# Kernel tuning notes

Hardware: AMD Instinct MI355X
Metric: run time of the kernel (lower is better)

The kernel has to match this reference:

```python
import jax, jax.numpy as jnp
import numpy as np

B, T, D, H = 2, 4096, 512, 8
DH = D // H  # dim_head = 64


def setup_inputs() -> dict:
    key = jax.random.key(0)
    ks = jax.random.split(key, 10)
    s = 1.0 / np.sqrt(D)
    x = jax.random.normal(ks[0], (B, T, D), dtype=jnp.float32)
    Wq = jax.random.uniform(ks[1], (D, D), jnp.float32, -s, s)
    Wk = jax.random.uniform(ks[2], (D, D), jnp.float32, -s, s)
    Wv = jax.random.uniform(ks[3], (D, D), jnp.float32, -s, s)
    Wo = jax.random.uniform(ks[4], (D, D), jnp.float32, -s, s)
    bq = jnp.zeros((D,), jnp.float32)
    bk = jnp.zeros((D,), jnp.float32)
    bv = jnp.zeros((D,), jnp.float32)
    bo = jnp.zeros((D,), jnp.float32)
    mask = jax.random.randint(ks[5], (1, 1, T, T), 0, 2).astype(bool)
    return {"x": x, "Wq": Wq, "bq": bq, "Wk": Wk, "bk": bk,
            "Wv": Wv, "bv": bv, "Wo": Wo, "bo": bo, "mask": mask}


def reference(x, Wq, bq, Wk, bk, Wv, bv, Wo, bo, mask):
    # QKV projections (self-attention: Q=K=V=x)
    def split_heads(t):
        return t.reshape(B, T, H, DH).transpose(0, 2, 1, 3)  # (B,H,T,DH)
    Q = split_heads(x @ Wq + bq)
    K = split_heads(x @ Wk + bk)
    V = split_heads(x @ Wv + bv)
    # scaled dot-product attention with additive mask penalty (as in source)
    scores = jnp.einsum('bhqd,bhkd->bhqk', Q, K) / np.sqrt(DH)
    scores = scores + (~mask).astype(scores.dtype) * (-1e9)
    att_w = jax.nn.softmax(scores, axis=-1)
    O = jnp.einsum('bhqk,bhkd->bhqd', att_w, V)
    O = O.transpose(0, 2, 1, 3).reshape(B, T, D)
    return O @ Wo + bo
```

## Files before the change

### kernel.cpp

```cpp
#include <hip/hip_runtime.h>
#include <stdint.h>

#define B_ 2
#define T_ 4096
#define D_ 512
#define H_ 8
#define DH_ 64

typedef __bf16 bf16;
typedef __bf16 bf16x4_t __attribute__((ext_vector_type(4)));
typedef __bf16 bf16x8_t __attribute__((ext_vector_type(8)));
typedef float f32x4 __attribute__((ext_vector_type(4)));
typedef uint32_t u32;

static constexpr float QSCALE = 0.18033688011112042f;

__device__ __forceinline__ void async16(void* lds, const void* g) {
  __builtin_amdgcn_global_load_lds(
      (const __attribute__((address_space(1))) void*)g,
      (__attribute__((address_space(3))) void*)lds, 16, 0, 0);
}

__global__ __launch_bounds__(256) void prep_kernel(
    const float* __restrict__ x,
    const float* __restrict__ Wq, const float* __restrict__ Wk,
    const float* __restrict__ Wv, const float* __restrict__ Wo,
    const void* __restrict__ maskp,
    bf16* __restrict__ xb, bf16* __restrict__ WTall, bf16* __restrict__ WoT,
    u32* __restrict__ bmask)
{
  int bid = blockIdx.x;
  int tid = threadIdx.x;
  if (bid < 4096) {
    int idx = bid * 256 + tid;
    const float4* xf = (const float4*)x;
    float4 v = xf[idx];
    bf16x4_t o;
    o[0] = (bf16)v.x; o[1] = (bf16)v.y; o[2] = (bf16)v.z; o[3] = (bf16)v.w;
    ((bf16x4_t*)xb)[idx] = o;
  } else if (bid < 8192) {
    int gid = (bid - 4096) * 256 + tid;
    int sel = gid >> 18;
    int idx = gid & 262143;
    int n = idx >> 9, k = idx & 511;
    if (sel < 3) {
      const float* W = (sel == 0) ? Wq : (sel == 1) ? Wk : Wv;
      float v = W[k * 512 + n];
      if (sel == 0) v *= QSCALE;
      WTall[gid] = (bf16)v;
    } else {
      WoT[idx] = (bf16)Wo[k * 512 + n];
    }
  } else {
    int wid = (bid - 8192) * 256 + tid;
    const uint8_t* m8 = (const uint8_t*)maskp;
    bool u8mode = (__ballot(m8[4 * (tid & 63) + 1] != 0) != 0ull);
    int row = wid >> 7, wcol = wid & 127;
    size_t off = (size_t)row * 4096 + (size_t)wcol * 32;
    u32 w = 0;
    if (u8mode) {
      const uint4* p = (const uint4*)(m8 + off);
      uint4 a = p[0], b = p[1];
      u32 ws[8] = {a.x, a.y, a.z, a.w, b.x, b.y, b.z, b.w};
      #pragma unroll
      for (int j = 0; j < 32; ++j)
        if ((ws[j >> 2] >> ((j & 3) * 8)) & 0xffu) w |= (1u << j);
    } else {
      const uint4* p = (const uint4*)((const u32*)maskp + off);
      #pragma unroll
      for (int q = 0; q < 8; ++q) {
        uint4 a = p[q];
        if (a.x) w |= 1u << (q * 4 + 0);
        if (a.y) w |= 1u << (q * 4 + 1);
        if (a.z) w |= 1u << (q * 4 + 2);
        if (a.w) w |= 1u << (q * 4 + 3);
      }
    }
    bmask[((size_t)(row >> 6) * 64 + (wcol >> 1)) * 128 + (row & 63) * 2 + (wcol & 1)] = w;
  }
}

__global__ __launch_bounds__(256) void qkv_kernel(
    const bf16* __restrict__ xb, const bf16* __restrict__ WTall,
    const float* __restrict__ bq, const float* __restrict__ bk,
    const float* __restrict__ bv,
    bf16* __restrict__ Qb, bf16* __restrict__ Kb, bf16* __restrict__ Vtb)
{
  __shared__ char smem[16384];
  char* smX = smem;
  char* smW = smem + 8192;
  int tid = threadIdx.x;
  int lane = tid & 63, wave = tid >> 6;
  int lo = lane & 15, quad = lane >> 4;
  int wr = wave >> 1, wc = wave & 1;
  int bm = blockIdx.x * 64;
  int bn = blockIdx.y * 64;
  int sel = bn >> 9;
  f32x4 acc[2][2] = {};
  for (int kc = 0; kc < 8; ++kc) {
    __syncthreads();
    for (int s = tid; s < 512; s += 256) {
      int row = s >> 3, slot = s & 7, cg = slot ^ (row & 7);
      async16(smX + s * 16, xb + (size_t)(bm + row) * 512 + kc * 64 + cg * 8);
      async16(smW + s * 16, WTall + (size_t)(bn + row) * 512 + kc * 64 + cg * 8);
    }
    __syncthreads();
    #pragma unroll
    for (int ks = 0; ks < 2; ++ks) {
      bf16x8_t a[2], b[2];
      #pragma unroll
      for (int mt = 0; mt < 2; ++mt) {
        int row = wr * 32 + mt * 16 + lo;
        int ch = (ks * 4 + quad) ^ (row & 7);
        a[mt] = *(const bf16x8_t*)(smX + row * 128 + ch * 16);
      }
      #pragma unroll
      for (int nt = 0; nt < 2; ++nt) {
        int row = wc * 32 + nt * 16 + lo;
        int ch = (ks * 4 + quad) ^ (row & 7);
        b[nt] = *(const bf16x8_t*)(smW + row * 128 + ch * 16);
      }
      if (sel == 2) {
        #pragma unroll
        for (int mt = 0; mt < 2; ++mt)
          #pragma unroll
          for (int nt = 0; nt < 2; ++nt)
            acc[mt][nt] = __builtin_amdgcn_mfma_f32_16x16x32_bf16(
                b[nt], a[mt], acc[mt][nt], 0, 0, 0);
      } else {
        #pragma unroll
        for (int mt = 0; mt < 2; ++mt)
          #pragma unroll
          for (int nt = 0; nt < 2; ++nt)
            acc[mt][nt] = __builtin_amdgcn_mfma_f32_16x16x32_bf16(
                a[mt], b[nt], acc[mt][nt], 0, 0, 0);
      }
    }
  }
  int b_ = bm >> 12;
  if (sel < 2) {
    #pragma unroll
    for (int mt = 0; mt < 2; ++mt) {
      #pragma unroll
      for (int nt = 0; nt < 2; ++nt) {
        int n0 = (bn + wc * 32 + nt * 16 + lo) & 511;
        int h = n0 >> 6, dh = n0 & 63;
        int m0 = bm + wr * 32 + mt * 16 + quad * 4;
        int t0 = m0 & 4095;
        float bias = (sel == 0) ? QSCALE * bq[n0] : bk[n0];
        bf16* dst = (sel == 0 ? Qb : Kb) + (size_t)(b_ * H_ + h) * T_ * DH_ + dh;
        #pragma unroll
        for (int r = 0; r < 4; ++r)
          dst[(size_t)(t0 + r) * 64] = (bf16)(acc[mt][nt][r] + bias);
      }
    }
  } else {
    #pragma unroll
    for (int mt = 0; mt < 2; ++mt) {
      #pragma unroll
      for (int nt = 0; nt < 2; ++nt) {
        int t0 = (bm & 4095) + wr * 32 + mt * 16 + lo;
        #pragma unroll
        for (int r = 0; r < 4; ++r) {
          int n0 = (bn & 511) + wc * 32 + nt * 16 + quad * 4 + r;
          float v = acc[mt][nt][r] + bv[n0];
          Vtb[((size_t)(b_ * H_ + (n0 >> 6)) * DH_ + (n0 & 63)) * T_ + t0] = (bf16)v;
        }
      }
    }
  }
}

__global__ __launch_bounds__(256, 4) void attn_kernel(
    const bf16* __restrict__ Qb, const bf16* __restrict__ Kb,
    const bf16* __restrict__ Vtb, const u32* __restrict__ bm2,
    bf16* __restrict__ Obuf)
{
  __shared__ char smem[27648];
  char* smK = smem;
  char* smV = smem + 8192;
  char* smP = smem + 16384;
  char* smM = smem + 26624;
  int tid = threadIdx.x;
  int lane = tid & 63, wave = tid >> 6;
  int lo = lane & 15, quad = lane >> 4;
  int qh = wave & 1, kh = wave >> 1;
  int bh = blockIdx.x >> 6;
  int qt = blockIdx.x & 63;
  int qbase = qt * 64;
  char* smPw = smP + wave * 2560;

  const bf16* Qg = Qb + ((size_t)bh * T_ + qbase + qh * 32) * DH_;
  bf16x8_t qf[2][2];
  #pragma unroll
  for (int mt = 0; mt < 2; ++mt)
    #pragma unroll
    for (int ks = 0; ks < 2; ++ks)
      qf[mt][ks] = *(const bf16x8_t*)(Qg + (mt * 16 + lo) * 64 + ks * 32 + quad * 8);

  f32x4 O[2][4] = {};
  float lsum[2][4] = {};

  const bf16* Kg = Kb + (size_t)bh * T_ * DH_;
  const bf16* Vg = Vtb + (size_t)bh * DH_ * T_;
  const u32* mg = bm2 + (size_t)qt * 8192;

  for (int kc = 0; kc < 64; ++kc) {
    __syncthreads();
    for (int s = tid; s < 512; s += 256) {
      int row = s >> 3, slot = s & 7, cg = slot ^ (row & 7);
      async16(smK + s * 16, Kg + (size_t)(kc * 64 + row) * 64 + cg * 8);
      async16(smV + s * 16, Vg + (size_t)row * T_ + kc * 64 + cg * 8);
    }
    if (tid < 128) ((u32*)smM)[tid] = mg[kc * 128 + tid];
    __syncthreads();
    f32x4 S[2][2] = {};
    #pragma unroll
    for (int ks = 0; ks < 2; ++ks)
      #pragma unroll
      for (int nt = 0; nt < 2; ++nt) {
        int key = kh * 32 + nt * 16 + lo;
        int ch = (ks * 4 + quad) ^ (key & 7);
        bf16x8_t kf = *(const bf16x8_t*)(smK + key * 128 + ch * 16);
        #pragma unroll
        for (int mt = 0; mt < 2; ++mt)
          S[mt][nt] = __builtin_amdgcn_mfma_f32_16x16x32_bf16(
              qf[mt][ks], kf, S[mt][nt], 0, 0, 0);
      }
    #pragma unroll
    for (int mt = 0; mt < 2; ++mt)
      #pragma unroll
      for (int r = 0; r < 4; ++r) {
        int q_l = qh * 32 + mt * 16 + quad * 4 + r;
        u32 w = (*(const u32*)(smM + (q_l * 2 + kh) * 4)) >> lo;
        int prow = mt * 16 + quad * 4 + r;
        #pragma unroll
        for (int nt = 0; nt < 2; ++nt) {
          float p = __builtin_amdgcn_exp2f(S[mt][nt][r]);
          p = ((w >> (nt * 16)) & 1u) ? p : 0.0f;
          lsum[mt][r] += p;
          *(bf16*)(smPw + prow * 80 + (nt * 16 + lo) * 2) = (bf16)p;
        }
      }
    bf16x8_t pf[2];
    #pragma unroll
    for (int mt = 0; mt < 2; ++mt)
      pf[mt] = *(const bf16x8_t*)(smPw + (mt * 16 + lo) * 80 + quad * 16);
    #pragma unroll
    for (int dt = 0; dt < 4; ++dt) {
      int d = dt * 16 + lo;
      int ch = (kh * 4 + quad) ^ (d & 7);
      bf16x8_t vf = *(const bf16x8_t*)(smV + d * 128 + ch * 16);
      #pragma unroll
      for (int mt = 0; mt < 2; ++mt)
        O[mt][dt] = __builtin_amdgcn_mfma_f32_16x16x32_bf16(
            pf[mt], vf, O[mt][dt], 0, 0, 0);
    }
  }
  #pragma unroll
  for (int mt = 0; mt < 2; ++mt)
    #pragma unroll
    for (int r = 0; r < 4; ++r) {
      float v = lsum[mt][r];
      v += __shfl_xor(v, 1); v += __shfl_xor(v, 2);
      v += __shfl_xor(v, 4); v += __shfl_xor(v, 8);
      lsum[mt][r] = v;
    }
  __syncthreads();
  float* smO = (float*)smem;
  float* smL = (float*)smP;
  if (kh == 1) {
    #pragma unroll
    for (int mt = 0; mt < 2; ++mt) {
      #pragma unroll
      for (int dt = 0; dt < 4; ++dt)
        #pragma unroll
        for (int r = 0; r < 4; ++r)
          smO[(qh * 32 + mt * 16 + quad * 4 + r) * 64 + dt * 16 + lo] = O[mt][dt][r];
      if (lo == 0)
        #pragma unroll
        for (int r = 0; r < 4; ++r)
          smL[qh * 32 + mt * 16 + quad * 4 + r] = lsum[mt][r];
    }
  }
  __syncthreads();
  if (kh == 0) {
    bf16* Og = Obuf + ((size_t)bh * T_ + qbase + qh * 32) * DH_;
    #pragma unroll
    for (int mt = 0; mt < 2; ++mt) {
      float inv[4];
      #pragma unroll
      for (int r = 0; r < 4; ++r) {
        int row = qh * 32 + mt * 16 + quad * 4 + r;
        inv[r] = 1.0f / (lsum[mt][r] + smL[row]);
      }
      #pragma unroll
      for (int dt = 0; dt < 4; ++dt)
        #pragma unroll
        for (int r = 0; r < 4; ++r) {
          int rl = mt * 16 + quad * 4 + r;
          float o = (O[mt][dt][r] + smO[(qh * 32 + rl) * 64 + dt * 16 + lo]) * inv[r];
          Og[(size_t)rl * 64 + dt * 16 + lo] = (bf16)o;
        }
    }
  }
}

__global__ __launch_bounds__(256) void proj_kernel(
    const bf16* __restrict__ Obuf, const bf16* __restrict__ WoT,
    const float* __restrict__ bo, float* __restrict__ out)
{
  __shared__ char smem[16384];
  char* smA = smem;
  char* smW = smem + 8192;
  int tid = threadIdx.x;
  int lane = tid & 63, wave = tid >> 6;
  int lo = lane & 15, quad = lane >> 4;
  int wr = wave >> 1, wc = wave & 1;
  int bm = blockIdx.x * 64;
  int bn = blockIdx.y * 64;
  int b_ = bm >> 12, trow = bm & 4095;
  f32x4 acc[2][2] = {};
  for (int kc = 0; kc < 8; ++kc) {
    __syncthreads();
    const bf16* Ag = Obuf + ((size_t)(b_ * H_ + kc) * T_ + trow) * DH_;
    for (int s = tid; s < 512; s += 256) {
      int row = s >> 3, slot = s & 7, cg = slot ^ (row & 7);
      async16(smA + s * 16, Ag + row * 64 + cg * 8);
      async16(smW + s * 16, WoT + (size_t)(bn + row) * 512 + kc * 64 + cg * 8);
    }
    __syncthreads();
    #pragma unroll
    for (int ks = 0; ks < 2; ++ks) {
      bf16x8_t a[2], b[2];
      #pragma unroll
      for (int mt = 0; mt < 2; ++mt) {
        int row = wr * 32 + mt * 16 + lo;
        int ch = (ks * 4 + quad) ^ (row & 7);
        a[mt] = *(const bf16x8_t*)(smA + row * 128 + ch * 16);
      }
      #pragma unroll
      for (int nt = 0; nt < 2; ++nt) {
        int row = wc * 32 + nt * 16 + lo;
        int ch = (ks * 4 + quad) ^ (row & 7);
        b[nt] = *(const bf16x8_t*)(smW + row * 128 + ch * 16);
      }
      #pragma unroll
      for (int mt = 0; mt < 2; ++mt)
        #pragma unroll
        for (int nt = 0; nt < 2; ++nt)
          acc[mt][nt] = __builtin_amdgcn_mfma_f32_16x16x32_bf16(
              a[mt], b[nt], acc[mt][nt], 0, 0, 0);
    }
  }
  #pragma unroll
  for (int mt = 0; mt < 2; ++mt) {
    #pragma unroll
    for (int nt = 0; nt < 2; ++nt) {
      int n_g = bn + wc * 32 + nt * 16 + lo;
      int m0 = bm + wr * 32 + mt * 16 + quad * 4;
      float bias = bo[n_g];
      #pragma unroll
      for (int r = 0; r < 4; ++r)
        out[(size_t)(m0 + r) * 512 + n_g] = acc[mt][nt][r] + bias;
    }
  }
}

extern "C" void kernel_launch(void* const* d_in, const int* in_sizes, int n_in,
                              void* d_out, int out_size, void* d_ws, size_t ws_size,
                              hipStream_t stream) {
  const float* x  = (const float*)d_in[0];
  const float* Wq = (const float*)d_in[1];
  const float* bq = (const float*)d_in[2];
  const float* Wk = (const float*)d_in[3];
  const float* bk = (const float*)d_in[4];
  const float* Wv = (const float*)d_in[5];
  const float* bv = (const float*)d_in[6];
  const float* Wo = (const float*)d_in[7];
  const float* bo = (const float*)d_in[8];
  const void* maskp = d_in[9];
  float* out = (float*)d_out;

  char* w = (char*)d_ws;
  bf16* xb    = (bf16*)(w);
  bf16* WTall = (bf16*)(w + 8388608);
  bf16* WoT   = (bf16*)(w + 9961472);
  bf16* Qb    = (bf16*)(w + 10485760);
  bf16* Kb    = (bf16*)(w + 18874368);
  bf16* Vtb   = (bf16*)(w + 27262976);
  bf16* Obuf  = (bf16*)(w + 35651584);
  u32*  bmask = (u32*)(w + 44040192);

  prep_kernel<<<10240, 256, 0, stream>>>(x, Wq, Wk, Wv, Wo, maskp,
                                         xb, WTall, WoT, bmask);
  qkv_kernel<<<dim3(128, 24), 256, 0, stream>>>(xb, WTall, bq, bk, bv,
                                                Qb, Kb, Vtb);
  attn_kernel<<<1024, 256, 0, stream>>>(Qb, Kb, Vtb, bmask, Obuf);
  proj_kernel<<<dim3(128, 8), 256, 0, stream>>>(Obuf, WoT, bo, out);
}
```

Before: 305.5 us.

## Keep attention probabilities in registers via transposed S; enlarge GEMM tiles to 128x128

The attention kernel now computes S transposed (K as the A operand), so each lane's exp results already sit in the layout the 16x16x16 MFMA expects for the P·V product. This removes the per-wave LDS round trip for P and makes the mask load asynchronous. Row-sum reduction and the cross-wave combine are reworked to match. The QKV and output projection GEMMs grow from 64x64 to 128x128 block tiles with 4x4 MFMA tiles per wave, which gives more reuse per load but launches fewer blocks and uses more registers.

```diff
diff --git a/kernel.cpp b/kernel.cpp
--- a/kernel.cpp
+++ b/kernel.cpp
@@ -11,6 +11,7 @@
 typedef __bf16 bf16x4_t __attribute__((ext_vector_type(4)));
 typedef __bf16 bf16x8_t __attribute__((ext_vector_type(8)));
 typedef float f32x4 __attribute__((ext_vector_type(4)));
+typedef short short4_t __attribute__((ext_vector_type(4)));
 typedef uint32_t u32;
 
 static constexpr float QSCALE = 0.18033688011112042f;
@@ -86,20 +87,20 @@
     const float* __restrict__ bv,
     bf16* __restrict__ Qb, bf16* __restrict__ Kb, bf16* __restrict__ Vtb)
 {
-  __shared__ char smem[16384];
+  __shared__ char smem[32768];
   char* smX = smem;
-  char* smW = smem + 8192;
+  char* smW = smem + 16384;
   int tid = threadIdx.x;
   int lane = tid & 63, wave = tid >> 6;
   int lo = lane & 15, quad = lane >> 4;
   int wr = wave >> 1, wc = wave & 1;
-  int bm = blockIdx.x * 64;
-  int bn = blockIdx.y * 64;
+  int bm = blockIdx.x * 128;
+  int bn = blockIdx.y * 128;
   int sel = bn >> 9;
-  f32x4 acc[2][2] = {};
+  f32x4 acc[4][4] = {};
   for (int kc = 0; kc < 8; ++kc) {
     __syncthreads();
-    for (int s = tid; s < 512; s += 256) {
+    for (int s = tid; s < 1024; s += 256) {
       int row = s >> 3, slot = s & 7, cg = slot ^ (row & 7);
       async16(smX + s * 16, xb + (size_t)(bm + row) * 512 + kc * 64 + cg * 8);
       async16(smW + s * 16, WTall + (size_t)(bn + row) * 512 + kc * 64 + cg * 8);
@@ -107,31 +108,31 @@
     __syncthreads();
     #pragma unroll
     for (int ks = 0; ks < 2; ++ks) {
-      bf16x8_t a[2], b[2];
-      #pragma unroll
-      for (int mt = 0; mt < 2; ++mt) {
-        int row = wr * 32 + mt * 16 + lo;
+      bf16x8_t a[4], b[4];
+      #pragma unroll
+      for (int mt = 0; mt < 4; ++mt) {
+        int row = wr * 64 + mt * 16 + lo;
         int ch = (ks * 4 + quad) ^ (row & 7);
         a[mt] = *(const bf16x8_t*)(smX + row * 128 + ch * 16);
       }
       #pragma unroll
-      for (int nt = 0; nt < 2; ++nt) {
-        int row = wc * 32 + nt * 16 + lo;
+      for (int nt = 0; nt < 4; ++nt) {
+        int row = wc * 64 + nt * 16 + lo;
         int ch = (ks * 4 + quad) ^ (row & 7);
         b[nt] = *(const bf16x8_t*)(smW + row * 128 + ch * 16);
       }
       if (sel == 2) {
         #pragma unroll
-        for (int mt = 0; mt < 2; ++mt)
+        for (int mt = 0; mt < 4; ++mt)
           #pragma unroll
-          for (int nt = 0; nt < 2; ++nt)
+          for (int nt = 0; nt < 4; ++nt)
             acc[mt][nt] = __builtin_amdgcn_mfma_f32_16x16x32_bf16(
                 b[nt], a[mt], acc[mt][nt], 0, 0, 0);
       } else {
         #pragma unroll
-        for (int mt = 0; mt < 2; ++mt)
+        for (int mt = 0; mt < 4; ++mt)
           #pragma unroll
-          for (int nt = 0; nt < 2; ++nt)
+          for (int nt = 0; nt < 4; ++nt)
             acc[mt][nt] = __builtin_amdgcn_mfma_f32_16x16x32_bf16(
                 a[mt], b[nt], acc[mt][nt], 0, 0, 0);
       }
@@ -140,12 +141,12 @@
   int b_ = bm >> 12;
   if (sel < 2) {
     #pragma unroll
-    for (int mt = 0; mt < 2; ++mt) {
-      #pragma unroll
-      for (int nt = 0; nt < 2; ++nt) {
-        int n0 = (bn + wc * 32 + nt * 16 + lo) & 511;
+    for (int mt = 0; mt < 4; ++mt) {
+      #pragma unroll
+      for (int nt = 0; nt < 4; ++nt) {
+        int n0 = (bn + wc * 64 + nt * 16 + lo) & 511;
         int h = n0 >> 6, dh = n0 & 63;
-        int m0 = bm + wr * 32 + mt * 16 + quad * 4;
+        int m0 = bm + wr * 64 + mt * 16 + quad * 4;
         int t0 = m0 & 4095;
         float bias = (sel == 0) ? QSCALE * bq[n0] : bk[n0];
         bf16* dst = (sel == 0 ? Qb : Kb) + (size_t)(b_ * H_ + h) * T_ * DH_ + dh;
@@ -156,13 +157,13 @@
     }
   } else {
     #pragma unroll
-    for (int mt = 0; mt < 2; ++mt) {
-      #pragma unroll
-      for (int nt = 0; nt < 2; ++nt) {
-        int t0 = (bm & 4095) + wr * 32 + mt * 16 + lo;
+    for (int mt = 0; mt < 4; ++mt) {
+      #pragma unroll
+      for (int nt = 0; nt < 4; ++nt) {
+        int t0 = (bm & 4095) + wr * 64 + mt * 16 + lo;
         #pragma unroll
         for (int r = 0; r < 4; ++r) {
-          int n0 = (bn & 511) + wc * 32 + nt * 16 + quad * 4 + r;
+          int n0 = (bn & 511) + wc * 64 + nt * 16 + quad * 4 + r;
           float v = acc[mt][nt][r] + bv[n0];
           Vtb[((size_t)(b_ * H_ + (n0 >> 6)) * DH_ + (n0 & 63)) * T_ + t0] = (bf16)v;
         }
@@ -176,34 +177,32 @@
     const bf16* __restrict__ Vtb, const u32* __restrict__ bm2,
     bf16* __restrict__ Obuf)
 {
-  __shared__ char smem[27648];
+  __shared__ char smem[16896];
   char* smK = smem;
   char* smV = smem + 8192;
-  char* smP = smem + 16384;
-  char* smM = smem + 26624;
+  u32* smM = (u32*)(smem + 16384);
   int tid = threadIdx.x;
   int lane = tid & 63, wave = tid >> 6;
   int lo = lane & 15, quad = lane >> 4;
   int qh = wave & 1, kh = wave >> 1;
   int bh = blockIdx.x >> 6;
-  int qt = blockIdx.x & 63;
-  int qbase = qt * 64;
-  char* smPw = smP + wave * 2560;
+  int qt64 = blockIdx.x & 63;
+  int qbase = qt64 * 64;
 
   const bf16* Qg = Qb + ((size_t)bh * T_ + qbase + qh * 32) * DH_;
   bf16x8_t qf[2][2];
   #pragma unroll
-  for (int mt = 0; mt < 2; ++mt)
+  for (int qt = 0; qt < 2; ++qt)
     #pragma unroll
     for (int ks = 0; ks < 2; ++ks)
-      qf[mt][ks] = *(const bf16x8_t*)(Qg + (mt * 16 + lo) * 64 + ks * 32 + quad * 8);
+      qf[qt][ks] = *(const bf16x8_t*)(Qg + (qt * 16 + lo) * 64 + ks * 32 + quad * 8);
 
   f32x4 O[2][4] = {};
-  float lsum[2][4] = {};
+  float lsum[2] = {0.f, 0.f};
 
   const bf16* Kg = Kb + (size_t)bh * T_ * DH_;
   const bf16* Vg = Vtb + (size_t)bh * DH_ * T_;
-  const u32* mg = bm2 + (size_t)qt * 8192;
+  const u32* mg = bm2 + (size_t)qt64 * 8192;
 
   for (int kc = 0; kc < 64; ++kc) {
     __syncthreads();
@@ -212,96 +211,95 @@
       async16(smK + s * 16, Kg + (size_t)(kc * 64 + row) * 64 + cg * 8);
       async16(smV + s * 16, Vg + (size_t)row * T_ + kc * 64 + cg * 8);
     }
-    if (tid < 128) ((u32*)smM)[tid] = mg[kc * 128 + tid];
-    __syncthreads();
-    f32x4 S[2][2] = {};
+    if (tid < 32) async16((char*)smM + tid * 16, mg + kc * 128 + tid * 4);
+    __syncthreads();
+    f32x4 St[2][2] = {};
     #pragma unroll
     for (int ks = 0; ks < 2; ++ks)
       #pragma unroll
-      for (int nt = 0; nt < 2; ++nt) {
-        int key = kh * 32 + nt * 16 + lo;
-        int ch = (ks * 4 + quad) ^ (key & 7);
-        bf16x8_t kf = *(const bf16x8_t*)(smK + key * 128 + ch * 16);
-        #pragma unroll
-        for (int mt = 0; mt < 2; ++mt)
-          S[mt][nt] = __builtin_amdgcn_mfma_f32_16x16x32_bf16(
-              qf[mt][ks], kf, S[mt][nt], 0, 0, 0);
-      }
-    #pragma unroll
-    for (int mt = 0; mt < 2; ++mt)
-      #pragma unroll
-      for (int r = 0; r < 4; ++r) {
-        int q_l = qh * 32 + mt * 16 + quad * 4 + r;
-        u32 w = (*(const u32*)(smM + (q_l * 2 + kh) * 4)) >> lo;
-        int prow = mt * 16 + quad * 4 + r;
-        #pragma unroll
-        for (int nt = 0; nt < 2; ++nt) {
-          float p = __builtin_amdgcn_exp2f(S[mt][nt][r]);
-          p = ((w >> (nt * 16)) & 1u) ? p : 0.0f;
-          lsum[mt][r] += p;
-          *(bf16*)(smPw + prow * 80 + (nt * 16 + lo) * 2) = (bf16)p;
+      for (int kt = 0; kt < 2; ++kt) {
+        int krow = kh * 32 + kt * 16 + lo;
+        int ch = (ks * 4 + quad) ^ (krow & 7);
+        bf16x8_t kf = *(const bf16x8_t*)(smK + krow * 128 + ch * 16);
+        #pragma unroll
+        for (int qt = 0; qt < 2; ++qt)
+          St[kt][qt] = __builtin_amdgcn_mfma_f32_16x16x32_bf16(
+              kf, qf[qt][ks], St[kt][qt], 0, 0, 0);
+      }
+    short4_t pf[2][2];
+    #pragma unroll
+    for (int qt = 0; qt < 2; ++qt) {
+      u32 w = smM[(qh * 32 + qt * 16 + lo) * 2 + kh] >> (quad * 4);
+      #pragma unroll
+      for (int kt = 0; kt < 2; ++kt) {
+        bf16x4_t t;
+        #pragma unroll
+        for (int r = 0; r < 4; ++r) {
+          float p = ((w >> (kt * 16 + r)) & 1u)
+                        ? __builtin_amdgcn_exp2f(St[kt][qt][r]) : 0.0f;
+          lsum[qt] += p;
+          t[r] = (bf16)p;
         }
-      }
-    bf16x8_t pf[2];
-    #pragma unroll
-    for (int mt = 0; mt < 2; ++mt)
-      pf[mt] = *(const bf16x8_t*)(smPw + (mt * 16 + lo) * 80 + quad * 16);
+        pf[qt][kt] = __builtin_bit_cast(short4_t, t);
+      }
+    }
     #pragma unroll
     for (int dt = 0; dt < 4; ++dt) {
       int d = dt * 16 + lo;
-      int ch = (kh * 4 + quad) ^ (d & 7);
-      bf16x8_t vf = *(const bf16x8_t*)(smV + d * 128 + ch * 16);
-      #pragma unroll
-      for (int mt = 0; mt < 2; ++mt)
-        O[mt][dt] = __builtin_amdgcn_mfma_f32_16x16x32_bf16(
-            pf[mt], vf, O[mt][dt], 0, 0, 0);
+      #pragma unroll
+      for (int kt = 0; kt < 2; ++kt) {
+        int c0 = kh * 4 + kt * 2 + (quad >> 1);
+        short4_t vf = *(const short4_t*)(
+            smV + d * 128 + ((c0 ^ (d & 7)) << 4) + ((quad & 1) << 3));
+        #pragma unroll
+        for (int qt = 0; qt < 2; ++qt)
+          O[qt][dt] = __builtin_amdgcn_mfma_f32_16x16x16bf16_1k(
+              pf[qt][kt], vf, O[qt][dt], 0, 0, 0);
+      }
     }
   }
   #pragma unroll
-  for (int mt = 0; mt < 2; ++mt)
-    #pragma unroll
-    for (int r = 0; r < 4; ++r) {
-      float v = lsum[mt][r];
-      v += __shfl_xor(v, 1); v += __shfl_xor(v, 2);
-      v += __shfl_xor(v, 4); v += __shfl_xor(v, 8);
-      lsum[mt][r] = v;
-    }
+  for (int qt = 0; qt < 2; ++qt) {
+    float v = lsum[qt];
+    v += __shfl_xor(v, 16);
+    v += __shfl_xor(v, 32);
+    lsum[qt] = v;
+  }
   __syncthreads();
   float* smO = (float*)smem;
-  float* smL = (float*)smP;
+  float* smL = (float*)(smem + 16384);
   if (kh == 1) {
     #pragma unroll
-    for (int mt = 0; mt < 2; ++mt) {
+    for (int qt = 0; qt < 2; ++qt) {
       #pragma unroll
       for (int dt = 0; dt < 4; ++dt)
         #pragma unroll
         for (int r = 0; r < 4; ++r)
-          smO[(qh * 32 + mt * 16 + quad * 4 + r) * 64 + dt * 16 + lo] = O[mt][dt][r];
-      if (lo == 0)
-        #pragma unroll
-        for (int r = 0; r < 4; ++r)
-          smL[qh * 32 + mt * 16 + quad * 4 + r] = lsum[mt][r];
-    }
+          smO[(qh * 32 + qt * 16 + quad * 4 + r) * 64 + dt * 16 + lo] = O[qt][dt][r];
+      if (quad == 0) smL[qh * 32 + qt * 16 + lo] = lsum[qt];
+    }
+  }
+  __syncthreads();
+  if (kh == 0 && quad == 0) {
+    #pragma unroll
+    for (int qt = 0; qt < 2; ++qt)
+      smL[qh * 32 + qt * 16 + lo] += lsum[qt];
   }
   __syncthreads();
   if (kh == 0) {
     bf16* Og = Obuf + ((size_t)bh * T_ + qbase + qh * 32) * DH_;
     #pragma unroll
-    for (int mt = 0; mt < 2; ++mt) {
-      float inv[4];
+    for (int qt = 0; qt < 2; ++qt) {
       #pragma unroll
       for (int r = 0; r < 4; ++r) {
-        int row = qh * 32 + mt * 16 + quad * 4 + r;
-        inv[r] = 1.0f / (lsum[mt][r] + smL[row]);
-      }
-      #pragma unroll
-      for (int dt = 0; dt < 4; ++dt)
-        #pragma unroll
-        for (int r = 0; r < 4; ++r) {
-          int rl = mt * 16 + quad * 4 + r;
-          float o = (O[mt][dt][r] + smO[(qh * 32 + rl) * 64 + dt * 16 + lo]) * inv[r];
+        int rl = qt * 16 + quad * 4 + r;
+        float inv = 1.0f / smL[qh * 32 + rl];
+        #pragma unroll
+        for (int dt = 0; dt < 4; ++dt) {
+          float o = (O[qt][dt][r] + smO[(qh * 32 + rl) * 64 + dt * 16 + lo]) * inv;
           Og[(size_t)rl * 64 + dt * 16 + lo] = (bf16)o;
         }
+      }
     }
   }
 }
@@ -310,21 +308,21 @@
     const bf16* __restrict__ Obuf, const bf16* __restrict__ WoT,
     const float* __restrict__ bo, float* __restrict__ out)
 {
-  __shared__ char smem[16384];
+  __shared__ char smem[32768];
   char* smA = smem;
-  char* smW = smem + 8192;
+  char* smW = smem + 16384;
   int tid = threadIdx.x;
   int lane = tid & 63, wave = tid >> 6;
   int lo = lane & 15, quad = lane >> 4;
   int wr = wave >> 1, wc = wave & 1;
-  int bm = blockIdx.x * 64;
-  int bn = blockIdx.y * 64;
+  int bm = blockIdx.x * 128;
+  int bn = blockIdx.y * 128;
   int b_ = bm >> 12, trow = bm & 4095;
-  f32x4 acc[2][2] = {};
+  f32x4 acc[4][4] = {};
   for (int kc = 0; kc < 8; ++kc) {
     __syncthreads();
     const bf16* Ag = Obuf + ((size_t)(b_ * H_ + kc) * T_ + trow) * DH_;
-    for (int s = tid; s < 512; s += 256) {
+    for (int s = tid; s < 1024; s += 256) {
       int row = s >> 3, slot = s & 7, cg = slot ^ (row & 7);
       async16(smA + s * 16, Ag + row * 64 + cg * 8);
       async16(smW + s * 16, WoT + (size_t)(bn + row) * 512 + kc * 64 + cg * 8);
@@ -332,33 +330,33 @@
     __syncthreads();
     #pragma unroll
     for (int ks = 0; ks < 2; ++ks) {
-      bf16x8_t a[2], b[2];
-      #pragma unroll
-      for (int mt = 0; mt < 2; ++mt) {
-        int row = wr * 32 + mt * 16 + lo;
+      bf16x8_t a[4], b[4];
+      #pragma unroll
+      for (int mt = 0; mt < 4; ++mt) {
+        int row = wr * 64 + mt * 16 + lo;
         int ch = (ks * 4 + quad) ^ (row & 7);
         a[mt] = *(const bf16x8_t*)(smA + row * 128 + ch * 16);
       }
       #pragma unroll
-      for (int nt = 0; nt < 2; ++nt) {
-        int row = wc * 32 + nt * 16 + lo;
+      for (int nt = 0; nt < 4; ++nt) {
+        int row = wc * 64 + nt * 16 + lo;
         int ch = (ks * 4 + quad) ^ (row & 7);
         b[nt] = *(const bf16x8_t*)(smW + row * 128 + ch * 16);
       }
       #pragma unroll
-      for (int mt = 0; mt < 2; ++mt)
-        #pragma unroll
-        for (int nt = 0; nt < 2; ++nt)
+      for (int mt = 0; mt < 4; ++mt)
+        #pragma unroll
+        for (int nt = 0; nt < 4; ++nt)
           acc[mt][nt] = __builtin_amdgcn_mfma_f32_16x16x32_bf16(
               a[mt], b[nt], acc[mt][nt], 0, 0, 0);
     }
   }
   #pragma unroll
-  for (int mt = 0; mt < 2; ++mt) {
-    #pragma unroll
-    for (int nt = 0; nt < 2; ++nt) {
-      int n_g = bn + wc * 32 + nt * 16 + lo;
-      int m0 = bm + wr * 32 + mt * 16 + quad * 4;
+  for (int mt = 0; mt < 4; ++mt) {
+    #pragma unroll
+    for (int nt = 0; nt < 4; ++nt) {
+      int n_g = bn + wc * 64 + nt * 16 + lo;
+      int m0 = bm + wr * 64 + mt * 16 + quad * 4;
       float bias = bo[n_g];
       #pragma unroll
       for (int r = 0; r < 4; ++r)
@@ -394,8 +392,8 @@
 
   prep_kernel<<<10240, 256, 0, stream>>>(x, Wq, Wk, Wv, Wo, maskp,
                                          xb, WTall, WoT, bmask);
-  qkv_kernel<<<dim3(128, 24), 256, 0, stream>>>(xb, WTall, bq, bk, bv,
-                                                Qb, Kb, Vtb);
+  qkv_kernel<<<dim3(64, 12), 256, 0, stream>>>(xb, WTall, bq, bk, bv,
+                                               Qb, Kb, Vtb);
   attn_kernel<<<1024, 256, 0, stream>>>(Qb, Kb, Vtb, bmask, Obuf);
-  proj_kernel<<<dim3(128, 8), 256, 0, stream>>>(Obuf, WoT, bo, out);
-}
+  proj_kernel<<<dim3(64, 4), 256, 0, stream>>>(Obuf, WoT, bo, out);
+}
```

Result: no change. 302.0 us (-1.2%).
